# Optimization experiments

Measured on AMD Instinct MI355X. Metric: run time of the kernel, lower is better.

The kernel has to match this reference:

```python
import jax, jax.numpy as jnp
import numpy as np

NV, NC = 4096, 16384        # n_vars, n_clauses
VL, CL = 8, 8               # vlabel_dim (ground_dim), clabel_dim
VE, CE = 128, 128           # vemb_dim, cemb_dim
ITERS = 4                   # max_iters
LN_EPS = 1e-5


def setup_inputs() -> dict:
    key = jax.random.key(0)
    ks = jax.random.split(key, 10)
    return {
        "vlabels": jax.random.normal(ks[0], (NV, VL), jnp.float32),
        "clabels": jax.random.normal(ks[1], (NC, CL), jnp.float32),
        "cmat_pos": jax.random.uniform(ks[2], (NC, NV), jnp.float32),
        "cmat_neg": jax.random.uniform(ks[3], (NC, NV), jnp.float32),
        "W_V_pos": jax.random.normal(ks[4], (VL + VE, CE), jnp.float32),
        "W_V_neg": jax.random.normal(ks[5], (VL + VE, CE), jnp.float32),
        "B_V": jax.random.normal(ks[6], (CE,), jnp.float32),
        "W_C_pos": jax.random.normal(ks[7], (CL + CE, VE), jnp.float32),
        "W_C_neg": jax.random.normal(ks[8], (CL + CE, VE), jnp.float32),
        "B_C": jax.random.normal(ks[9], (VE,), jnp.float32),
        "ln_gamma": jnp.ones((VE,), jnp.float32),
        "ln_beta": jnp.zeros((VE,), jnp.float32),
    }


def _layernorm(x, gamma, beta):
    mu = jnp.mean(x, axis=-1, keepdims=True)
    var = jnp.var(x, axis=-1, keepdims=True)
    return (x - mu) * jax.lax.rsqrt(var + LN_EPS) * gamma + beta


def reference(vlabels, clabels, cmat_pos, cmat_neg,
              W_V_pos, W_V_neg, B_V, W_C_pos, W_C_neg, B_C,
              ln_gamma, ln_beta):
    n_vars = vlabels.shape[0]
    vmat_pos = cmat_pos.T  # [NV, NC]
    vmat_neg = cmat_neg.T
    vembs0 = jnp.zeros((n_vars, VE), vlabels.dtype)

    def step(vembs, _):
        vs = jnp.concatenate([vlabels, vembs], axis=1)          # [NV, VL+VE]
        pv = vs @ W_V_pos                                       # [NV, CE]
        nv = vs @ W_V_neg
        cembs = jax.nn.relu(cmat_pos @ pv + cmat_neg @ nv + B_V)  # [NC, CE]
        cs = jnp.concatenate([clabels, cembs], axis=1)          # [NC, CL+CE]
        pc = cs @ W_C_pos                                       # [NC, VE]
        nc = cs @ W_C_neg
        v = jax.nn.relu(vmat_pos @ pc + vmat_neg @ nc + B_C)    # [NV, VE]
        v = _layernorm(v, ln_gamma, ln_beta)
        return v, None

    vembs, _ = jax.lax.scan(step, vembs0, None, length=ITERS)
    return vembs
```

## Files before the change

### kernel.cpp

```cpp
#include <hip/hip_runtime.h>

#define NVV 4096
#define NCC 16384

typedef __attribute__((ext_vector_type(8))) short short8;
typedef __attribute__((ext_vector_type(4))) short short4v;
typedef __attribute__((ext_vector_type(4))) float f32x4;

__device__ __forceinline__ short f2bf(float f) {
  union { float f; unsigned u; } v; v.f = f;
  unsigned r = v.u + 0x7fffu + ((v.u >> 16) & 1u);
  return (short)(r >> 16);
}

template<typename AT>
__device__ __forceinline__ short8 load8v(const AT* p) {
  if constexpr (sizeof(AT) == 2) {
    return *(const short8*)p;
  } else {
    const f32x4* q = (const f32x4*)p;
    f32x4 a = q[0], b = q[1];
    short8 o;
#pragma unroll
    for (int j = 0; j < 4; ++j) { o[j] = f2bf(a[j]); o[j + 4] = f2bf(b[j]); }
    return o;
  }
}

__global__ __launch_bounds__(256) void k_conv(const float* __restrict__ src,
                                              short* __restrict__ dst, int n8) {
  int i = blockIdx.x * blockDim.x + threadIdx.x;
  const int stride = gridDim.x * blockDim.x;
  for (; i < n8; i += stride) {
    const f32x4* q = (const f32x4*)(src + (size_t)i * 8);
    f32x4 a = q[0], b = q[1];
    short8 o;
#pragma unroll
    for (int j = 0; j < 4; ++j) { o[j] = f2bf(a[j]); o[j + 4] = f2bf(b[j]); }
    *(short8*)(dst + (size_t)i * 8) = o;
  }
}

__global__ __launch_bounds__(256) void k_convT(const float* __restrict__ src,
                                               short* __restrict__ dstN,
                                               short* __restrict__ dstT,
                                               int R, int C) {
  __shared__ short t[64][66];
  const int r0 = blockIdx.y * 64, c0 = blockIdx.x * 64;
  const int tr = threadIdx.x >> 2;
  const int q  = (threadIdx.x & 3) << 4;
  const float* s = src + (size_t)(r0 + tr) * C + c0 + q;
  const f32x4 v0 = *(const f32x4*)(s);
  const f32x4 v1 = *(const f32x4*)(s + 4);
  const f32x4 v2 = *(const f32x4*)(s + 8);
  const f32x4 v3 = *(const f32x4*)(s + 12);
  short8 a, b;
#pragma unroll
  for (int j = 0; j < 4; ++j) {
    a[j] = f2bf(v0[j]); a[4 + j] = f2bf(v1[j]);
    b[j] = f2bf(v2[j]); b[4 + j] = f2bf(v3[j]);
  }
  short* dn = dstN + (size_t)(r0 + tr) * C + c0 + q;
  *(short8*)dn = a;
  *(short8*)(dn + 8) = b;
#pragma unroll
  for (int j = 0; j < 8; ++j) { t[tr][q + j] = a[j]; t[tr][q + 8 + j] = b[j]; }
  __syncthreads();
  short8 oa, ob;
#pragma unroll
  for (int j = 0; j < 8; ++j) { oa[j] = t[q + j][tr]; ob[j] = t[q + 8 + j][tr]; }
  short* dt = dstT + (size_t)(c0 + tr) * R + r0 + q;
  *(short8*)dt = oa;
  *(short8*)(dt + 8) = ob;
}

template<int SRC, int NROW>
__global__ __launch_bounds__(128) void k_mlp(
    const float* __restrict__ labels, const float* __restrict__ embs,
    const float* __restrict__ bias,
    const float* __restrict__ Wp, const float* __restrict__ Wn,
    short* __restrict__ Tp, short* __restrict__ Tn, int Nrows, int KS) {
  __shared__ float xs[NROW][130];
  const int n = threadIdx.x;
  const int m0 = blockIdx.x * NROW;
  if (SRC == 2) {
#pragma unroll
    for (int r = 0; r < NROW; ++r) {
      const size_t m = m0 + r;
      float v = bias[n];
      for (int ks = 0; ks < KS; ++ks)
        v += embs[((size_t)ks * NCC + m) * 128 + n];
      xs[r][n] = fmaxf(v, 0.f);
    }
    __syncthreads();
  }
  float ap[NROW] = {}, an[NROW] = {};
  const int JMAX = (SRC == 0) ? 8 : 136;
  for (int j = 0; j < JMAX; ++j) {
    const float wp = Wp[j * 128 + n], wn = Wn[j * 128 + n];
#pragma unroll
    for (int r = 0; r < NROW; ++r) {
      float x;
      if (j < 8)            x = labels[(size_t)(m0 + r) * 8 + j];
      else if (SRC == 2)    x = xs[r][j - 8];
      else                  x = embs[(size_t)(m0 + r) * 128 + (j - 8)];
      ap[r] = fmaf(x, wp, ap[r]);
      an[r] = fmaf(x, wn, an[r]);
    }
  }
  short8 vp0, vn0, vp1, vn1;
#pragma unroll
  for (int r = 0; r < 8; ++r) {
    vp0[r] = f2bf(ap[r]); vn0[r] = f2bf(an[r]);
    vp1[r] = f2bf(ap[8 + r]); vn1[r] = f2bf(an[8 + r]);
  }
  *(short8*)(Tp + (size_t)n * Nrows + m0) = vp0;
  *(short8*)(Tp + (size_t)n * Nrows + m0 + 8) = vp1;
  *(short8*)(Tn + (size_t)n * Nrows + m0) = vn0;
  *(short8*)(Tn + (size_t)n * Nrows + m0 + 8) = vn1;
}

__global__ __launch_bounds__(256, 3) void k_gemm5(
    const short* __restrict__ Ap, const short* __restrict__ An,
    const short* __restrict__ Bp, const short* __restrict__ Bn,
    float* __restrict__ C, int M, int lda, int ldb, int Klen) {
  __shared__ __align__(16) short sA[2][4096];
  __shared__ __align__(16) short sB[2][8192];
  const int tid = threadIdx.x;
  const int w = tid >> 6, l = tid & 63, lr = l & 15, lh = l >> 4;
  const int wr = w >> 1, wc = w & 1;
  const int m0 = blockIdx.x * 64;
  const int Koff = (int)blockIdx.z * Klen;
  const int T = Klen >> 6;

  const int srow = tid >> 3;
  const int scol = ((tid & 7) ^ (srow & 7)) << 3;
  const short* gA0 = Ap + (size_t)(m0 + srow) * lda + Koff + scol;
  const short* gA1 = An + (size_t)(m0 + srow) * lda + Koff + scol;
  const short* gB0 = Bp + (size_t)srow * ldb + Koff + scol;
  const short* gB1 = Bn + (size_t)srow * ldb + Koff + scol;

  f32x4 acc[2][4] = {};

  for (int step = 0; step < T; ++step) {
    const int k0 = step << 6;
#pragma unroll
    for (int i = 0; i < 2; ++i) {
      const size_t ra = (size_t)(i * 32) * lda + k0;
      const int ld = i * 2048 + w * 512;
      __builtin_amdgcn_global_load_lds(
          (const __attribute__((address_space(1))) void*)(gA0 + ra),
          (__attribute__((address_space(3))) void*)(&sA[0][ld]), 16, 0, 0);
      __builtin_amdgcn_global_load_lds(
          (const __attribute__((address_space(1))) void*)(gA1 + ra),
          (__attribute__((address_space(3))) void*)(&sA[1][ld]), 16, 0, 0);
    }
#pragma unroll
    for (int i = 0; i < 4; ++i) {
      const size_t rb = (size_t)(i * 32) * ldb + k0;
      const int ld = i * 2048 + w * 512;
      __builtin_amdgcn_global_load_lds(
          (const __attribute__((address_space(1))) void*)(gB0 + rb),
          (__attribute__((address_space(3))) void*)(&sB[0][ld]), 16, 0, 0);
      __builtin_amdgcn_global_load_lds(
          (const __attribute__((address_space(1))) void*)(gB1 + rb),
          (__attribute__((address_space(3))) void*)(&sB[1][ld]), 16, 0, 0);
    }
    __syncthreads();
#pragma unroll
    for (int kk = 0; kk < 2; ++kk) {
#pragma unroll
      for (int mat = 0; mat < 2; ++mat) {
        const int kc = (kk << 2) + lh;
        short8 a[2], b[4];
#pragma unroll
        for (int mi = 0; mi < 2; ++mi) {
          const int row = (wr << 5) + (mi << 4) + lr;
          a[mi] = *(const short8*)&sA[mat][(row << 6) + ((kc ^ (row & 7)) << 3)];
        }
#pragma unroll
        for (int nj = 0; nj < 4; ++nj) {
          const int n = (wc << 6) + (nj << 4) + lr;
          b[nj] = *(const short8*)&sB[mat][(n << 6) + ((kc ^ (n & 7)) << 3)];
        }
#pragma unroll
        for (int mi = 0; mi < 2; ++mi)
#pragma unroll
          for (int nj = 0; nj < 4; ++nj)
            acc[mi][nj] = __builtin_amdgcn_mfma_f32_16x16x32_bf16(
                a[mi], b[nj], acc[mi][nj], 0, 0, 0);
      }
    }
    __syncthreads();
  }

  const size_t crow0 = (size_t)blockIdx.z * M + m0 + (wr << 5) + (lh << 2);
#pragma unroll
  for (int mi = 0; mi < 2; ++mi)
#pragma unroll
    for (int nj = 0; nj < 4; ++nj) {
      const int col = (wc << 6) + (nj << 4) + lr;
#pragma unroll
      for (int r = 0; r < 4; ++r)
        C[(crow0 + (mi << 4) + r) * 128 + col] = acc[mi][nj][r];
    }
}

template<typename AT, bool TRANSA, int EPI>
__global__ __launch_bounds__(256) void k_gemm(
    const AT* __restrict__ Ap, const AT* __restrict__ An,
    const short* __restrict__ Bp, const short* __restrict__ Bn,
    const float* __restrict__ bias, float* __restrict__ C,
    int M, int lda, int ldb, int Klen) {
  __shared__ __align__(16) short sA[2][32 * 64];
  __shared__ __align__(16) short sB[2][64 * 64];
  const int tid = threadIdx.x;
  const int w = tid >> 6, l = tid & 63, lr = l & 15, lh = l >> 4;
  const int m0 = blockIdx.x * 32, n0 = blockIdx.y * 64;
  const int Koff = blockIdx.z * Klen;
  f32x4 acc0 = {0.f, 0.f, 0.f, 0.f}, acc1 = {0.f, 0.f, 0.f, 0.f};

  for (int step = 0; step < (Klen >> 6); ++step) {
    const int k0 = Koff + (step << 6);
    __syncthreads();
    if (!TRANSA) {
      const int m = tid >> 3, kc = tid & 7;
      const size_t ga = (size_t)(m0 + m) * lda + k0 + (kc << 3);
      const int ad = (m << 6) + ((kc ^ (m & 7)) << 3);
      *(short8*)&sA[0][ad] = load8v(Ap + ga);
      *(short8*)&sA[1][ad] = load8v(An + ga);
    } else {
      const int r = tid >> 2, c8 = (tid & 3) << 3;
      const size_t ga = (size_t)(k0 + r) * lda + m0 + c8;
      short8 vp = load8v(Ap + ga), vn = load8v(An + ga);
#pragma unroll
      for (int j = 0; j < 8; ++j) {
        const int m = c8 + j;
        const int ad = (m << 6) + ((((r >> 3)) ^ (m & 7)) << 3) + (r & 7);
        sA[0][ad] = vp[j];
        sA[1][ad] = vn[j];
      }
    }
#pragma unroll
    for (int i = 0; i < 2; ++i) {
      const int c = (i << 8) + tid;
      const int n = c >> 3, kc = c & 7;
      const size_t gb = (size_t)(n0 + n) * ldb + k0 + (kc << 3);
      const int ad = (n << 6) + ((kc ^ (n & 7)) << 3);
      *(short8*)&sB[0][ad] = *(const short8*)(Bp + gb);
      *(short8*)&sB[1][ad] = *(const short8*)(Bn + gb);
    }
    __syncthreads();
#pragma unroll
    for (int kh = 0; kh < 2; ++kh) {
      const int kc = (kh << 2) + lh;
      const int bn_ = (w << 4) + lr;
      short8 bp = *(short8*)&sB[0][(bn_ << 6) + ((kc ^ (bn_ & 7)) << 3)];
      short8 bnv = *(short8*)&sB[1][(bn_ << 6) + ((kc ^ (bn_ & 7)) << 3)];
      short8 a0p = *(short8*)&sA[0][(lr << 6) + ((kc ^ (lr & 7)) << 3)];
      short8 a0n = *(short8*)&sA[1][(lr << 6) + ((kc ^ (lr & 7)) << 3)];
      const int m1 = 16 + lr;
      short8 a1p = *(short8*)&sA[0][(m1 << 6) + ((kc ^ (m1 & 7)) << 3)];
      short8 a1n = *(short8*)&sA[1][(m1 << 6) + ((kc ^ (m1 & 7)) << 3)];
      acc0 = __builtin_amdgcn_mfma_f32_16x16x32_bf16(a0p, bp, acc0, 0, 0, 0);
      acc0 = __builtin_amdgcn_mfma_f32_16x16x32_bf16(a0n, bnv, acc0, 0, 0, 0);
      acc1 = __builtin_amdgcn_mfma_f32_16x16x32_bf16(a1p, bp, acc1, 0, 0, 0);
      acc1 = __builtin_amdgcn_mfma_f32_16x16x32_bf16(a1n, bnv, acc1, 0, 0, 0);
    }
  }
  const int n = n0 + (w << 4) + lr;
#pragma unroll
  for (int mf = 0; mf < 2; ++mf) {
    f32x4 a = mf ? acc1 : acc0;
#pragma unroll
    for (int r = 0; r < 4; ++r) {
      const int m = m0 + (mf << 4) + (lh << 2) + r;
      float c = a[r];
      if (EPI == 0) {
        c += bias[n];
        c = fmaxf(c, 0.f);
        C[(size_t)m * 128 + n] = c;
      } else {
        C[((size_t)blockIdx.z * M + m) * 128 + n] = c;
      }
    }
  }
}

template<int KS>
__global__ __launch_bounds__(256) void k_reduce_ln(
    const float* __restrict__ part, const float* __restrict__ bias,
    const float* __restrict__ gamma, const float* __restrict__ beta,
    float* __restrict__ out) {
  const int w = threadIdx.x >> 6, l = threadIdx.x & 63;
  const int m = blockIdx.x * 4 + w;
  const int n0 = l << 1;
  float x0 = bias[n0], x1 = bias[n0 + 1];
#pragma unroll
  for (int ks = 0; ks < KS; ++ks) {
    const size_t o = ((size_t)ks * NVV + m) * 128 + n0;
    x0 += part[o];
    x1 += part[o + 1];
  }
  x0 = fmaxf(x0, 0.f);
  x1 = fmaxf(x1, 0.f);
  float s = x0 + x1, q = x0 * x0 + x1 * x1;
#pragma unroll
  for (int off = 32; off; off >>= 1) {
    s += __shfl_xor(s, off);
    q += __shfl_xor(q, off);
  }
  const float mu = s * (1.f / 128.f);
  const float var = q * (1.f / 128.f) - mu * mu;
  const float inv = 1.f / sqrtf(var + 1e-5f);
  out[(size_t)m * 128 + n0]     = (x0 - mu) * inv * gamma[n0] + beta[n0];
  out[(size_t)m * 128 + n0 + 1] = (x1 - mu) * inv * gamma[n0 + 1] + beta[n0 + 1];
}

extern "C" void kernel_launch(void* const* d_in, const int* in_sizes, int n_in,
                              void* d_out, int out_size, void* d_ws, size_t ws_size,
                              hipStream_t stream) {
  const float* vlabels  = (const float*)d_in[0];
  const float* clabels  = (const float*)d_in[1];
  const float* cmat_pos = (const float*)d_in[2];
  const float* cmat_neg = (const float*)d_in[3];
  const float* Wvp = (const float*)d_in[4];
  const float* Wvn = (const float*)d_in[5];
  const float* Bv  = (const float*)d_in[6];
  const float* Wcp = (const float*)d_in[7];
  const float* Wcn = (const float*)d_in[8];
  const float* Bc  = (const float*)d_in[9];
  const float* gam = (const float*)d_in[10];
  const float* bet = (const float*)d_in[11];
  float* out = (float*)d_out;

  char* base = (char*)d_ws;
  const size_t SZ_vT  = (size_t)128 * NVV * 2;
  const size_t SZ_cT  = (size_t)128 * NCC * 2;
  const size_t SZ_cm  = (size_t)NCC * NVV * 2;
  const size_t SZ_p8  = (size_t)NCC * 128 * 4;

  size_t o = 0;
  auto al = [&](size_t b) { size_t p = o; o += (b + 255) & ~(size_t)255; return p; };
  short* pvT  = (short*)(base + al(SZ_vT));
  short* nvT  = (short*)(base + al(SZ_vT));
  short* pcT  = (short*)(base + al(SZ_cT));
  short* ncT  = (short*)(base + al(SZ_cT));
  short* cmPb = (short*)(base + al(SZ_cm));
  short* cmNb = (short*)(base + al(SZ_cm));
  short* cmTP = (short*)(base + al(SZ_cm));
  short* cmTN = (short*)(base + al(SZ_cm));
  float* part = (float*)(base + al(4 * SZ_p8));
  const size_t needFA = o;
  const size_t needFB = needFA - 2 * SZ_p8;

  const bool fastA = ws_size >= needFA;
  const bool fastB = !fastA && ws_size >= needFB;

  if (fastA || fastB) {
    const int SK1 = fastA ? 4 : 2;
    const int SK2 = fastA ? 16 : 8;
    k_convT<<<dim3(NVV / 64, NCC / 64), 256, 0, stream>>>(cmat_pos, cmPb, cmTP, NCC, NVV);
    k_convT<<<dim3(NVV / 64, NCC / 64), 256, 0, stream>>>(cmat_neg, cmNb, cmTN, NCC, NVV);

    for (int it = 0; it < 4; ++it) {
      if (it == 0)
        k_mlp<0, 16><<<NVV / 16, 128, 0, stream>>>(vlabels, nullptr, nullptr, Wvp, Wvn, pvT, nvT, NVV, 0);
      else
        k_mlp<1, 16><<<NVV / 16, 128, 0, stream>>>(vlabels, out, nullptr, Wvp, Wvn, pvT, nvT, NVV, 0);

      k_gemm5<<<dim3(NCC / 64, 1, SK1), 256, 0, stream>>>(
          cmPb, cmNb, pvT, nvT, part, NCC, NVV, NVV, NVV / SK1);
      k_mlp<2, 16><<<NCC / 16, 128, 0, stream>>>(clabels, part, Bv, Wcp, Wcn, pcT, ncT, NCC, SK1);

      k_gemm5<<<dim3(NVV / 64, 1, SK2), 256, 0, stream>>>(
          cmTP, cmTN, pcT, ncT, part, NVV, NCC, NCC, NCC / SK2);
      if (fastA)
        k_reduce_ln<16><<<NVV / 4, 256, 0, stream>>>(part, Bc, gam, bet, out);
      else
        k_reduce_ln<8><<<NVV / 4, 256, 0, stream>>>(part, Bc, gam, bet, out);
    }
    return;
  }

  o = 0;
  pvT  = (short*)(base + al(SZ_vT));
  nvT  = (short*)(base + al(SZ_vT));
  pcT  = (short*)(base + al(SZ_cT));
  ncT  = (short*)(base + al(SZ_cT));
  part = (float*)(base + al(2 * SZ_p8));
  float* cemb = (float*)(base + al(SZ_p8));
  cmPb = (short*)(base + al(SZ_cm));
  cmNb = (short*)(base + al(SZ_cm));
  const size_t needN = o;
  const bool big = ws_size >= needN;

  if (big) {
    k_conv<<<4096, 256, 0, stream>>>(cmat_pos, cmPb, NCC * NVV / 8);
    k_conv<<<4096, 256, 0, stream>>>(cmat_neg, cmNb, NCC * NVV / 8);
  }

  for (int it = 0; it < 4; ++it) {
    if (it == 0)
      k_mlp<0, 16><<<NVV / 16, 128, 0, stream>>>(vlabels, nullptr, nullptr, Wvp, Wvn, pvT, nvT, NVV, 0);
    else
      k_mlp<1, 16><<<NVV / 16, 128, 0, stream>>>(vlabels, out, nullptr, Wvp, Wvn, pvT, nvT, NVV, 0);

    if (big) {
      k_gemm5<<<dim3(NCC / 64, 1, 2), 256, 0, stream>>>(
          cmPb, cmNb, pvT, nvT, part, NCC, NVV, NVV, NVV / 2);
      k_mlp<2, 16><<<NCC / 16, 128, 0, stream>>>(clabels, part, Bv, Wcp, Wcn, pcT, ncT, NCC, 2);
      k_gemm<short, true, 1><<<dim3(NVV / 32, 2, 4), 256, 0, stream>>>(
          cmPb, cmNb, pcT, ncT, nullptr, part, NVV, NVV, NCC, NVV);
      k_reduce_ln<4><<<NVV / 4, 256, 0, stream>>>(part, Bc, gam, bet, out);
    } else {
      k_gemm<float, false, 0><<<dim3(NCC / 32, 2, 1), 256, 0, stream>>>(
          cmat_pos, cmat_neg, pvT, nvT, Bv, cemb, NCC, NVV, NVV, NVV);
      k_mlp<1, 16><<<NCC / 16, 128, 0, stream>>>(clabels, cemb, nullptr, Wcp, Wcn, pcT, ncT, NCC, 0);
      k_gemm<float, true, 1><<<dim3(NVV / 32, 2, 4), 256, 0, stream>>>(
          cmat_pos, cmat_neg, pcT, ncT, nullptr, part, NVV, NVV, NCC, NVV);
      k_reduce_ln<4><<<NVV / 4, 256, 0, stream>>>(part, Bc, gam, bet, out);
    }
  }
}
```

Measured before the change: 1.536 ms.

## Replace split-K GEMM with 4-stage LDS-pipelined kernel and fused bias-relu epilogue

Replaces k_gemm5 with k_gemm6, which streams the pos and neg operand halves as alternating K-stages through a 4-buffer LDS ring. Loads are issued two stages ahead and waited on with vmcnt counters instead of full __syncthreads pairs. The first GEMM no longer splits K, so bias+ReLU are applied in its epilogue and the separate partial-sum reduction in k_mlp<2> goes away. The second GEMM drops split-K from 16 to 4, with block ids folded into a 1D grid. Fewer split-K slices cut partial-sum traffic but leave far fewer blocks (256 for the first GEMM) on a large GPU, and occupancy falls to 1 block per CU.

```diff
diff --git a/kernel.cpp b/kernel.cpp
--- a/kernel.cpp
+++ b/kernel.cpp
@@ -2,6 +2,8 @@
 
 #define NVV 4096
 #define NCC 16384
+#define AS1 __attribute__((address_space(1)))
+#define AS3 __attribute__((address_space(3)))
 
 typedef __attribute__((ext_vector_type(8))) short short8;
 typedef __attribute__((ext_vector_type(4))) short short4v;
@@ -120,89 +122,95 @@
   *(short8*)(Tn + (size_t)n * Nrows + m0 + 8) = vn1;
 }
 
-__global__ __launch_bounds__(256, 3) void k_gemm5(
+template<int EPI, int LSK>
+__global__ __launch_bounds__(256, 1) void k_gemm6(
     const short* __restrict__ Ap, const short* __restrict__ An,
     const short* __restrict__ Bp, const short* __restrict__ Bn,
-    float* __restrict__ C, int M, int lda, int ldb, int Klen) {
-  __shared__ __align__(16) short sA[2][4096];
-  __shared__ __align__(16) short sB[2][8192];
+    const float* __restrict__ bias, float* __restrict__ C,
+    int M, int lda, int ldb, int Klen) {
+  __shared__ __align__(16) short sb[4][12288];
   const int tid = threadIdx.x;
   const int w = tid >> 6, l = tid & 63, lr = l & 15, lh = l >> 4;
   const int wr = w >> 1, wc = w & 1;
-  const int m0 = blockIdx.x * 64;
-  const int Koff = (int)blockIdx.z * Klen;
-  const int T = Klen >> 6;
+  const int id = blockIdx.x;
+  const int zw = id & ((1 << LSK) - 1);
+  const int xw = id >> LSK;
+  const int m0 = xw * 64;
+  const int Koff = zw * Klen;
+  const int T = (Klen >> 6) << 1;
 
   const int srow = tid >> 3;
   const int scol = ((tid & 7) ^ (srow & 7)) << 3;
-  const short* gA0 = Ap + (size_t)(m0 + srow) * lda + Koff + scol;
-  const short* gA1 = An + (size_t)(m0 + srow) * lda + Koff + scol;
-  const short* gB0 = Bp + (size_t)srow * ldb + Koff + scol;
-  const short* gB1 = Bn + (size_t)srow * ldb + Koff + scol;
+  const short* gAp = Ap + (size_t)(m0 + srow) * lda + Koff + scol;
+  const short* gAn = An + (size_t)(m0 + srow) * lda + Koff + scol;
+  const short* gBp = Bp + (size_t)srow * ldb + Koff + scol;
+  const short* gBn = Bn + (size_t)srow * ldb + Koff + scol;
 
   f32x4 acc[2][4] = {};
 
-  for (int step = 0; step < T; ++step) {
-    const int k0 = step << 6;
-#pragma unroll
-    for (int i = 0; i < 2; ++i) {
-      const size_t ra = (size_t)(i * 32) * lda + k0;
-      const int ld = i * 2048 + w * 512;
+  auto stage = [&](int t, int buf) {
+    const int tt = (t < T) ? t : t - T;
+    const int k0 = (tt >> 1) << 6;
+    const short* A = (tt & 1) ? gAn : gAp;
+    const short* B = (tt & 1) ? gBn : gBp;
+#pragma unroll
+    for (int i = 0; i < 2; ++i)
       __builtin_amdgcn_global_load_lds(
-          (const __attribute__((address_space(1))) void*)(gA0 + ra),
-          (__attribute__((address_space(3))) void*)(&sA[0][ld]), 16, 0, 0);
+          (const AS1 void*)(A + (size_t)(i * 32) * lda + k0),
+          (AS3 void*)(&sb[buf][i * 2048 + w * 512]), 16, 0, 0);
+#pragma unroll
+    for (int i = 0; i < 4; ++i)
       __builtin_amdgcn_global_load_lds(
-          (const __attribute__((address_space(1))) void*)(gA1 + ra),
-          (__attribute__((address_space(3))) void*)(&sA[1][ld]), 16, 0, 0);
-    }
-#pragma unroll
-    for (int i = 0; i < 4; ++i) {
-      const size_t rb = (size_t)(i * 32) * ldb + k0;
-      const int ld = i * 2048 + w * 512;
-      __builtin_amdgcn_global_load_lds(
-          (const __attribute__((address_space(1))) void*)(gB0 + rb),
-          (__attribute__((address_space(3))) void*)(&sB[0][ld]), 16, 0, 0);
-      __builtin_amdgcn_global_load_lds(
-          (const __attribute__((address_space(1))) void*)(gB1 + rb),
-          (__attribute__((address_space(3))) void*)(&sB[1][ld]), 16, 0, 0);
-    }
-    __syncthreads();
+          (const AS1 void*)(B + (size_t)(i * 32) * ldb + k0),
+          (AS3 void*)(&sb[buf][4096 + i * 2048 + w * 512]), 16, 0, 0);
+  };
+
+  stage(0, 0);
+  stage(1, 1);
+
+  for (int t = 0; t < T; ++t) {
+    stage(t + 2, (t + 2) & 3);
+    asm volatile("s_waitcnt vmcnt(12)" ::: "memory");
+    __builtin_amdgcn_s_barrier();
+    asm volatile("" ::: "memory");
+    const short* bp = &sb[t & 3][0];
 #pragma unroll
     for (int kk = 0; kk < 2; ++kk) {
-#pragma unroll
-      for (int mat = 0; mat < 2; ++mat) {
-        const int kc = (kk << 2) + lh;
-        short8 a[2], b[4];
-#pragma unroll
-        for (int mi = 0; mi < 2; ++mi) {
-          const int row = (wr << 5) + (mi << 4) + lr;
-          a[mi] = *(const short8*)&sA[mat][(row << 6) + ((kc ^ (row & 7)) << 3)];
-        }
-#pragma unroll
-        for (int nj = 0; nj < 4; ++nj) {
-          const int n = (wc << 6) + (nj << 4) + lr;
-          b[nj] = *(const short8*)&sB[mat][(n << 6) + ((kc ^ (n & 7)) << 3)];
-        }
-#pragma unroll
-        for (int mi = 0; mi < 2; ++mi)
-#pragma unroll
-          for (int nj = 0; nj < 4; ++nj)
-            acc[mi][nj] = __builtin_amdgcn_mfma_f32_16x16x32_bf16(
-                a[mi], b[nj], acc[mi][nj], 0, 0, 0);
+      const int kc = (kk << 2) + lh;
+      short8 a[2], b[4];
+#pragma unroll
+      for (int mi = 0; mi < 2; ++mi) {
+        const int row = (wr << 5) + (mi << 4) + lr;
+        a[mi] = *(const short8*)&bp[(row << 6) + ((kc ^ (row & 7)) << 3)];
       }
-    }
-    __syncthreads();
-  }
-
-  const size_t crow0 = (size_t)blockIdx.z * M + m0 + (wr << 5) + (lh << 2);
+#pragma unroll
+      for (int nj = 0; nj < 4; ++nj) {
+        const int n = (wc << 6) + (nj << 4) + lr;
+        b[nj] = *(const short8*)&bp[4096 + (n << 6) + ((kc ^ (n & 7)) << 3)];
+      }
+#pragma unroll
+      for (int mi = 0; mi < 2; ++mi)
+#pragma unroll
+        for (int nj = 0; nj < 4; ++nj)
+          acc[mi][nj] = __builtin_amdgcn_mfma_f32_16x16x32_bf16(
+              a[mi], b[nj], acc[mi][nj], 0, 0, 0);
+    }
+  }
+
 #pragma unroll
   for (int mi = 0; mi < 2; ++mi)
 #pragma unroll
     for (int nj = 0; nj < 4; ++nj) {
       const int col = (wc << 6) + (nj << 4) + lr;
 #pragma unroll
-      for (int r = 0; r < 4; ++r)
-        C[(crow0 + (mi << 4) + r) * 128 + col] = acc[mi][nj][r];
+      for (int r = 0; r < 4; ++r) {
+        const int m = m0 + (wr << 5) + (mi << 4) + (lh << 2) + r;
+        if (EPI == 0) {
+          C[(size_t)m * 128 + col] = fmaxf(acc[mi][nj][r] + bias[col], 0.f);
+        } else {
+          C[((size_t)zw * M + m) * 128 + col] = acc[mi][nj][r];
+        }
+      }
     }
 }
 
@@ -255,16 +263,16 @@
     for (int kh = 0; kh < 2; ++kh) {
       const int kc = (kh << 2) + lh;
       const int bn_ = (w << 4) + lr;
-      short8 bp = *(short8*)&sB[0][(bn_ << 6) + ((kc ^ (bn_ & 7)) << 3)];
+      short8 bpv = *(short8*)&sB[0][(bn_ << 6) + ((kc ^ (bn_ & 7)) << 3)];
       short8 bnv = *(short8*)&sB[1][(bn_ << 6) + ((kc ^ (bn_ & 7)) << 3)];
       short8 a0p = *(short8*)&sA[0][(lr << 6) + ((kc ^ (lr & 7)) << 3)];
       short8 a0n = *(short8*)&sA[1][(lr << 6) + ((kc ^ (lr & 7)) << 3)];
       const int m1 = 16 + lr;
       short8 a1p = *(short8*)&sA[0][(m1 << 6) + ((kc ^ (m1 & 7)) << 3)];
       short8 a1n = *(short8*)&sA[1][(m1 << 6) + ((kc ^ (m1 & 7)) << 3)];
-      acc0 = __builtin_amdgcn_mfma_f32_16x16x32_bf16(a0p, bp, acc0, 0, 0, 0);
+      acc0 = __builtin_amdgcn_mfma_f32_16x16x32_bf16(a0p, bpv, acc0, 0, 0, 0);
       acc0 = __builtin_amdgcn_mfma_f32_16x16x32_bf16(a0n, bnv, acc0, 0, 0, 0);
-      acc1 = __builtin_amdgcn_mfma_f32_16x16x32_bf16(a1p, bp, acc1, 0, 0, 0);
+      acc1 = __builtin_amdgcn_mfma_f32_16x16x32_bf16(a1p, bpv, acc1, 0, 0, 0);
       acc1 = __builtin_amdgcn_mfma_f32_16x16x32_bf16(a1n, bnv, acc1, 0, 0, 0);
     }
   }
@@ -335,31 +343,26 @@
   float* out = (float*)d_out;
 
   char* base = (char*)d_ws;
-  const size_t SZ_vT  = (size_t)128 * NVV * 2;
-  const size_t SZ_cT  = (size_t)128 * NCC * 2;
-  const size_t SZ_cm  = (size_t)NCC * NVV * 2;
-  const size_t SZ_p8  = (size_t)NCC * 128 * 4;
+  const size_t SZ_vT = (size_t)128 * NVV * 2;
+  const size_t SZ_cT = (size_t)128 * NCC * 2;
+  const size_t SZ_cm = (size_t)NCC * NVV * 2;
+  const size_t SZ_p8 = (size_t)NCC * 128 * 4;
 
   size_t o = 0;
   auto al = [&](size_t b) { size_t p = o; o += (b + 255) & ~(size_t)255; return p; };
+
   short* pvT  = (short*)(base + al(SZ_vT));
   short* nvT  = (short*)(base + al(SZ_vT));
   short* pcT  = (short*)(base + al(SZ_cT));
   short* ncT  = (short*)(base + al(SZ_cT));
+  float* scr8 = (float*)(base + al(SZ_p8));
   short* cmPb = (short*)(base + al(SZ_cm));
   short* cmNb = (short*)(base + al(SZ_cm));
   short* cmTP = (short*)(base + al(SZ_cm));
   short* cmTN = (short*)(base + al(SZ_cm));
-  float* part = (float*)(base + al(4 * SZ_p8));
-  const size_t needFA = o;
-  const size_t needFB = needFA - 2 * SZ_p8;
-
-  const bool fastA = ws_size >= needFA;
-  const bool fastB = !fastA && ws_size >= needFB;
-
-  if (fastA || fastB) {
-    const int SK1 = fastA ? 4 : 2;
-    const int SK2 = fastA ? 16 : 8;
+  const size_t needF = o;
+
+  if (ws_size >= needF) {
     k_convT<<<dim3(NVV / 64, NCC / 64), 256, 0, stream>>>(cmat_pos, cmPb, cmTP, NCC, NVV);
     k_convT<<<dim3(NVV / 64, NCC / 64), 256, 0, stream>>>(cmat_neg, cmNb, cmTN, NCC, NVV);
 
@@ -369,26 +372,25 @@
       else
         k_mlp<1, 16><<<NVV / 16, 128, 0, stream>>>(vlabels, out, nullptr, Wvp, Wvn, pvT, nvT, NVV, 0);
 
-      k_gemm5<<<dim3(NCC / 64, 1, SK1), 256, 0, stream>>>(
-          cmPb, cmNb, pvT, nvT, part, NCC, NVV, NVV, NVV / SK1);
-      k_mlp<2, 16><<<NCC / 16, 128, 0, stream>>>(clabels, part, Bv, Wcp, Wcn, pcT, ncT, NCC, SK1);
-
-      k_gemm5<<<dim3(NVV / 64, 1, SK2), 256, 0, stream>>>(
-          cmTP, cmTN, pcT, ncT, part, NVV, NCC, NCC, NCC / SK2);
-      if (fastA)
-        k_reduce_ln<16><<<NVV / 4, 256, 0, stream>>>(part, Bc, gam, bet, out);
-      else
-        k_reduce_ln<8><<<NVV / 4, 256, 0, stream>>>(part, Bc, gam, bet, out);
+      k_gemm6<0, 0><<<NCC / 64, 256, 0, stream>>>(
+          cmPb, cmNb, pvT, nvT, Bv, scr8, NCC, NVV, NVV, NVV);
+
+      k_mlp<1, 16><<<NCC / 16, 128, 0, stream>>>(clabels, scr8, nullptr, Wcp, Wcn, pcT, ncT, NCC, 0);
+
+      k_gemm6<1, 2><<<(NVV / 64) * 4, 256, 0, stream>>>(
+          cmTP, cmTN, pcT, ncT, nullptr, scr8, NVV, NCC, NCC, NCC / 4);
+
+      k_reduce_ln<4><<<NVV / 4, 256, 0, stream>>>(scr8, Bc, gam, bet, out);
     }
     return;
   }
 
   o = 0;
-  pvT  = (short*)(base + al(SZ_vT));
-  nvT  = (short*)(base + al(SZ_vT));
-  pcT  = (short*)(base + al(SZ_cT));
-  ncT  = (short*)(base + al(SZ_cT));
-  part = (float*)(base + al(2 * SZ_p8));
+  pvT = (short*)(base + al(SZ_vT));
+  nvT = (short*)(base + al(SZ_vT));
+  pcT = (short*)(base + al(SZ_cT));
+  ncT = (short*)(base + al(SZ_cT));
+  float* part = (float*)(base + al(2 * SZ_p8));
   float* cemb = (float*)(base + al(SZ_p8));
   cmPb = (short*)(base + al(SZ_cm));
   cmNb = (short*)(base + al(SZ_cm));
@@ -407,9 +409,9 @@
       k_mlp<1, 16><<<NVV / 16, 128, 0, stream>>>(vlabels, out, nullptr, Wvp, Wvn, pvT, nvT, NVV, 0);
 
     if (big) {
-      k_gemm5<<<dim3(NCC / 64, 1, 2), 256, 0, stream>>>(
-          cmPb, cmNb, pvT, nvT, part, NCC, NVV, NVV, NVV / 2);
-      k_mlp<2, 16><<<NCC / 16, 128, 0, stream>>>(clabels, part, Bv, Wcp, Wcn, pcT, ncT, NCC, 2);
+      k_gemm<short, false, 0><<<dim3(NCC / 32, 2, 1), 256, 0, stream>>>(
+          cmPb, cmNb, pvT, nvT, Bv, cemb, NCC, NVV, NVV, NVV);
+      k_mlp<1, 16><<<NCC / 16, 128, 0, stream>>>(clabels, cemb, nullptr, Wcp, Wcn, pcT, ncT, NCC, 0);
       k_gemm<short, true, 1><<<dim3(NVV / 32, 2, 4), 256, 0, stream>>>(
           cmPb, cmNb, pcT, ncT, nullptr, part, NVV, NVV, NCC, NVV);
       k_reduce_ln<4><<<NVV / 4, 256, 0, stream>>>(part, Bc, gam, bet, out);
```

Result: faster. 1.382 ms (-10.1%).
